# Performance work log

Hardware: AMD Instinct MI355X
Metric: run time of the kernel (lower is better)

The kernel has to match this reference:

```python
import jax, jax.numpy as jnp
import numpy as np

B, A, C, D = 64, 1024, 64, 512
NEG = -9.0e15


def _ln(x, w, b, eps=1e-5):
    mu = jnp.mean(x, axis=-1, keepdims=True)
    var = jnp.mean((x - mu) ** 2, axis=-1, keepdims=True)
    return (x - mu) * jax.lax.rsqrt(var + eps) * w + b


def setup_inputs() -> dict:
    key = jax.random.key(0)
    ks = jax.random.split(key, 8)
    att_index = np.arange(A) % C
    am = np.zeros((C, A), np.float32)
    am[att_index, np.arange(A)] = 1.0 / (A // C)  # avgmask[i,j]=1/count if att_index[j]==i
    adj_ha = np.concatenate([am, np.eye(C, dtype=np.float32)], axis=1)      # [C, A+C]
    adj_ah = np.concatenate([am.T, np.eye(A, dtype=np.float32)], axis=1)    # [A, C+A]
    w = lambda k: jax.random.normal(k, (D, D), jnp.float32) * 0.05
    ones, zeros = jnp.ones((D,), jnp.float32), jnp.zeros((D,), jnp.float32)
    return {
        "att_vf": jax.random.normal(ks[0], (B, A, D), jnp.float32) * 0.05,
        "avgmask": jnp.asarray(am), "adj_ha": jnp.asarray(adj_ha), "adj_ah": jnp.asarray(adj_ah),
        "l1_W_h2h": w(ks[1]), "l1_W_h2a": w(ks[2]),
        "l1_ln1_w": ones, "l1_ln1_b": zeros, "l1_ln2_w": ones, "l1_ln2_b": zeros,
        "l1_ln3_w": ones, "l1_ln3_b": zeros,
        "l2_W_a2h": w(ks[3]), "l2_W_h2h": w(ks[4]), "l2_W_h2a": w(ks[5]),
        "l2_ln1_w": ones, "l2_ln1_b": zeros, "l2_ln2_w": ones, "l2_ln2_b": zeros,
        "l2_ln3_w": ones, "l2_ln3_b": zeros,
    }


def _forward(att_vf, avgmask, adj_ha, adj_ah,
             l1_W_h2h, l1_W_h2a, l1_ln1_w, l1_ln1_b, l1_ln2_w, l1_ln2_b, l1_ln3_w, l1_ln3_b,
             l2_W_a2h, l2_W_h2h, l2_W_h2a, l2_ln1_w, l2_ln1_b, l2_ln2_w, l2_ln2_b, l2_ln3_w, l2_ln3_b):
    inv_sd = 1.0 / jnp.sqrt(jnp.float32(D))  # input_dim == h_dim == D

    def h2h(hl, W, lw, lb):
        hln = _ln(hl, lw, lb)                                  # [B,C,D]
        hide = hln @ W
        s = jnp.einsum('bid,bjd->bij', hide, hide) * inv_sd
        a = jax.nn.softmax(s, axis=-1)
        return jnp.einsum('bij,bjd->bid', a, hln)

    def h2a(upd_hl, att, W, lw, lb):
        hln = _ln(upd_hl, lw, lb)
        hidden = jnp.concatenate([hln @ W, att], axis=1)       # [B, C+A, D]
        s = jnp.einsum('bad,bkd->bak', att, hidden) * inv_sd   # [B, A, C+A]
        s = jnp.where(adj_ah > 0, s, NEG)
        a = jax.nn.softmax(s, axis=-1)
        return jnp.einsum('bak,bkd->bad', a, hidden)

    # layer 1: a2h = 'avg'
    hl = jnp.einsum('ca,bad->bcd', avgmask, _ln(att_vf, l1_ln1_w, l1_ln1_b))  # [B,C,D]
    hl1 = h2h(hl, l1_W_h2h, l1_ln2_w, l1_ln2_b)
    att1 = h2a(hl1, att_vf, l1_W_h2a, l1_ln3_w, l1_ln3_b)

    # layer 2: a2h = 'attention'
    att_ln = _ln(att1, l2_ln1_w, l2_ln1_b)
    hidden = jnp.concatenate([att_ln @ l2_W_a2h, hl1], axis=1)  # [B, A+C, D]
    s = jnp.einsum('bcd,bkd->bck', hl1, hidden) * inv_sd        # [B, C, A+C]
    s = jnp.where(adj_ha > 0, s, NEG)
    hl2 = jnp.einsum('bck,bkd->bcd', jax.nn.softmax(s, axis=-1), hidden)
    hl2 = h2h(hl2, l2_W_h2h, l2_ln2_w, l2_ln2_b)
    att2 = h2a(hl2, att1, l2_W_h2a, l2_ln3_w, l2_ln3_b)
    return att2


def reference(att_vf, avgmask, adj_ha, adj_ah,
              l1_W_h2h, l1_W_h2a, l1_ln1_w, l1_ln1_b, l1_ln2_w, l1_ln2_b, l1_ln3_w, l1_ln3_b,
              l2_W_a2h, l2_W_h2h, l2_W_h2a, l2_ln1_w, l2_ln1_b, l2_ln2_w, l2_ln2_b, l2_ln3_w, l2_ln3_b):
    return _forward(att_vf, avgmask, adj_ha, adj_ah,
                    l1_W_h2h, l1_W_h2a, l1_ln1_w, l1_ln1_b, l1_ln2_w, l1_ln2_b, l1_ln3_w, l1_ln3_b,
                    l2_W_a2h, l2_W_h2h, l2_W_h2a, l2_ln1_w, l2_ln1_b, l2_ln2_w, l2_ln2_b, l2_ln3_w, l2_ln3_b)
```

## Files before the change

kernel.cpp:

```cpp
#include <hip/hip_runtime.h>

#define B_ 64
#define A_ 1024
#define C_ 64
#define D_ 512
#define INV_SD 0.044194173824159216f

typedef __bf16 bf16_t;
typedef __bf16 bf16x8 __attribute__((ext_vector_type(8)));
typedef __bf16 bf16x2 __attribute__((ext_vector_type(2)));
typedef float f32x4 __attribute__((ext_vector_type(4)));

static __device__ __forceinline__ bf16_t f2b(float x) { return (bf16_t)x; }
static __device__ __forceinline__ float b2f(bf16_t x) { return (float)x; }

static __device__ __forceinline__ void gl_lds16(const void* g, void* l) {
  __builtin_amdgcn_global_load_lds(
      (const __attribute__((address_space(1))) unsigned int*)g,
      (__attribute__((address_space(3))) unsigned int*)l, 16, 0, 0);
}

__global__ __launch_bounds__(256) void k_prep(const float* __restrict__ att,
                                              const float* __restrict__ lw1,
                                              const float* __restrict__ lb1,
                                              const float* __restrict__ lw2,
                                              const float* __restrict__ lb2,
                                              bf16_t* __restrict__ hlnb,
                                              const float* __restrict__ W0,
                                              const float* __restrict__ W1,
                                              const float* __restrict__ W2,
                                              const float* __restrict__ W3,
                                              const float* __restrict__ W4,
                                              bf16_t* __restrict__ WtBase) {
  __shared__ float shm[64 * 65];
  __shared__ float reds[8];
  int bid = blockIdx.x;
  int t = threadIdx.x;
  if (bid < B_ * C_) {
    int b = bid >> 6, c = bid & 63;
    int w = t >> 6, lane = t & 63;
    float (*part)[512] = (float(*)[512])shm;
    float ps[8] = {0.f, 0.f, 0.f, 0.f, 0.f, 0.f, 0.f, 0.f};
#pragma unroll
    for (int i = 0; i < 4; ++i) {
      int jj = w * 4 + i;
      const float* xr = att + ((size_t)b * A_ + jj * 64 + c) * D_ + lane * 8;
      float4 v1 = *(const float4*)xr;
      float4 v2 = *(const float4*)(xr + 4);
      float v[8] = {v1.x, v1.y, v1.z, v1.w, v2.x, v2.y, v2.z, v2.w};
      float s = 0.f, q = 0.f;
#pragma unroll
      for (int u = 0; u < 8; ++u) { s += v[u]; q += v[u] * v[u]; }
#pragma unroll
      for (int o = 32; o; o >>= 1) { s += __shfl_xor(s, o); q += __shfl_xor(q, o); }
      float mu = s * (1.0f / D_);
      float rs = rsqrtf(q * (1.0f / D_) - mu * mu + 1e-5f);
#pragma unroll
      for (int u = 0; u < 8; ++u) ps[u] += (v[u] - mu) * rs;
    }
#pragma unroll
    for (int u = 0; u < 8; ++u) part[w][lane * 8 + u] = ps[u];
    __syncthreads();
    int d = 2 * t;
    float hx = ((part[0][d] + part[1][d]) + (part[2][d] + part[3][d])) * (1.f / 16.f) * lw1[d] + lb1[d];
    float hy = ((part[0][d + 1] + part[1][d + 1]) + (part[2][d + 1] + part[3][d + 1])) * (1.f / 16.f) * lw1[d + 1] + lb1[d + 1];
    float s = hx + hy, q = hx * hx + hy * hy;
#pragma unroll
    for (int o = 32; o; o >>= 1) { s += __shfl_xor(s, o); q += __shfl_xor(q, o); }
    if (lane == 0) { reds[w] = s; reds[4 + w] = q; }
    __syncthreads();
    float S = (reds[0] + reds[1]) + (reds[2] + reds[3]);
    float Q = (reds[4] + reds[5]) + (reds[6] + reds[7]);
    float mu = S * (1.0f / D_);
    float rs = rsqrtf(Q * (1.0f / D_) - mu * mu + 1e-5f);
    bf16x2 ob;
    ob.x = f2b((hx - mu) * rs * lw2[d] + lb2[d]);
    ob.y = f2b((hy - mu) * rs * lw2[d + 1] + lb2[d + 1]);
    *(bf16x2*)(hlnb + (size_t)bid * D_ + d) = ob;
  } else {
    int idx = bid - B_ * C_;
    int z = idx >> 6;
    int rem = idx & 63;
    int k0 = (rem & 7) * 64, n0 = (rem >> 3) * 64;
    const float* Ws[5] = {W0, W1, W2, W3, W4};
    int r0 = t >> 6;
    int c = t & 63;
    if (z == 5) {
      const float* W = Ws[2];
      bf16_t* Wt = WtBase + (size_t)5 * 512 * 512;
#pragma unroll 4
      for (int i = 0; i < 16; ++i) {
        int r = r0 * 16 + i;
        Wt[(size_t)(k0 + r) * 512 + n0 + c] = f2b(W[(size_t)(k0 + r) * 512 + n0 + c]);
      }
      return;
    }
    const float* W = Ws[z];
    bf16_t* Wt = WtBase + (size_t)z * 512 * 512;
    float (*tile)[65] = (float(*)[65])shm;
#pragma unroll 4
    for (int i = 0; i < 16; ++i) {
      int r = r0 * 16 + i;
      tile[r][c] = W[(size_t)(k0 + r) * 512 + n0 + c];
    }
    __syncthreads();
#pragma unroll 4
    for (int i = 0; i < 16; ++i) {
      int r = r0 * 16 + i;
      Wt[(size_t)(n0 + r) * 512 + k0 + c] = f2b(tile[c][r]);
    }
  }
}

__global__ __launch_bounds__(256) void k_ln_tr(const bf16_t* __restrict__ x,
                                               const float* __restrict__ lw,
                                               const float* __restrict__ lb,
                                               bf16_t* __restrict__ y,
                                               bf16_t* __restrict__ yt) {
  __shared__ bf16_t lnS[64][528];
  int b = blockIdx.x;
  int t = threadIdx.x;
  int wv = t >> 6, lane = t & 63;
  int d0 = lane * 8;
  float4 w1 = *(const float4*)(lw + d0);
  float4 w2 = *(const float4*)(lw + d0 + 4);
  float4 b1 = *(const float4*)(lb + d0);
  float4 b2 = *(const float4*)(lb + d0 + 4);
  float lwv[8] = {w1.x, w1.y, w1.z, w1.w, w2.x, w2.y, w2.z, w2.w};
  float lbv[8] = {b1.x, b1.y, b1.z, b1.w, b2.x, b2.y, b2.z, b2.w};
  const bf16_t* xb = x + (size_t)b * C_ * D_;
  bf16_t* yb = y + (size_t)b * C_ * D_;
#pragma unroll 4
  for (int i = 0; i < 16; ++i) {
    int r = wv * 16 + i;
    bf16x8 xv = *(const bf16x8*)(xb + (size_t)r * D_ + d0);
    float v[8], s = 0.f, q = 0.f;
#pragma unroll
    for (int u = 0; u < 8; ++u) { v[u] = b2f(xv[u]); s += v[u]; q += v[u] * v[u]; }
#pragma unroll
    for (int o = 32; o; o >>= 1) { s += __shfl_xor(s, o); q += __shfl_xor(q, o); }
    float mu = s * (1.0f / D_);
    float rs = rsqrtf(q * (1.0f / D_) - mu * mu + 1e-5f);
    bf16x8 ob;
#pragma unroll
    for (int u = 0; u < 8; ++u) ob[u] = f2b((v[u] - mu) * rs * lwv[u] + lbv[u]);
    *(bf16x8*)(yb + (size_t)r * D_ + d0) = ob;
    *(bf16x8*)(&lnS[r][d0]) = ob;
  }
  __syncthreads();
  bf16_t* tb = yt + (size_t)b * D_ * C_;
#pragma unroll
  for (int pass = 0; pass < 16; ++pass) {
    int d = pass * 32 + (t >> 3);
    int c0 = (t & 7) * 8;
    unsigned short tmp[8];
#pragma unroll
    for (int u = 0; u < 8; ++u) tmp[u] = *(const unsigned short*)&lnS[c0 + u][d];
    *(uint4*)(tb + (size_t)d * 64 + c0) = *(const uint4*)tmp;
  }
}

template <bool BIAS>
__global__ __launch_bounds__(256, 4) void k_gemm64(const bf16_t* __restrict__ A0,
                                                   const bf16_t* __restrict__ W0,
                                                   bf16_t* __restrict__ C0,
                                                   const bf16_t* __restrict__ A1,
                                                   const bf16_t* __restrict__ W1,
                                                   bf16_t* __restrict__ C1,
                                                   const bf16_t* __restrict__ Rb,
                                                   int tiles_per, int ntiles,
                                                   const bf16_t* __restrict__ trS,
                                                   bf16_t* __restrict__ trD) {
  constexpr int ABYTES = 64 * 128;
  constexpr int BUF = 2 * ABYTES;
  __shared__ char smem[2 * BUF];

  int t = threadIdx.x;
  int bid = blockIdx.x;

  if (bid >= ntiles) {
    int idx = bid - ntiles;
    int n0 = idx & 7, b = idx >> 3;
    unsigned short(*sm)[72] = (unsigned short(*)[72])smem;
    const bf16_t* sb = trS + (size_t)b * C_ * D_;
    bf16_t* db = trD + (size_t)b * D_ * C_;
#pragma unroll
    for (int rep = 0; rep < 2; ++rep) {
      int f = t + rep * 256;
      int r = f >> 3, c8 = f & 7;
      uint4 v = *(const uint4*)(sb + (size_t)r * D_ + n0 * 64 + c8 * 8);
      unsigned int* p = (unsigned int*)&sm[r][c8 * 8];
      p[0] = v.x; p[1] = v.y; p[2] = v.z; p[3] = v.w;
    }
    __syncthreads();
#pragma unroll
    for (int rep = 0; rep < 2; ++rep) {
      int f = t + rep * 256;
      int nr = f >> 3, c8 = f & 7;
      unsigned short tmp[8];
#pragma unroll
      for (int u = 0; u < 8; ++u) tmp[u] = sm[c8 * 8 + u][nr];
      *(uint4*)(db + (size_t)(n0 * 64 + nr) * 64 + c8 * 8) = *(const uint4*)tmp;
    }
    return;
  }

  int lane = t & 63, wave = t >> 6;
  int wr = wave >> 1, wc = wave & 1;
  int lhi = lane >> 4, llo = lane & 15;

  int tile = (bid & 7) * (ntiles >> 3) + (bid >> 3);
  int sel = (tile >= tiles_per) ? 1 : 0;
  int tidx = tile - sel * tiles_per;
  int bm = tidx >> 3, bn = tidx & 7;

  const bf16_t* Ab = (sel ? A1 : A0) + (size_t)bm * 64 * 512;
  const bf16_t* Wb = (sel ? W1 : W0) + (size_t)bn * 64 * 512;
  bf16_t* Cmat = sel ? C1 : C0;

  int l3 = lane >> 3;
  int srcOff = ((lane & 7) ^ l3) * 8;

  auto stage = [&](int k0, int bi) {
    char* As = smem + bi * BUF;
    char* Bs = As + ABYTES;
#pragma unroll
    for (int i = 0; i < 2; ++i) {
      int r0 = wave * 16 + i * 8;
      gl_lds16(Ab + (size_t)(r0 + l3) * 512 + k0 + srcOff, As + r0 * 128);
      gl_lds16(Wb + (size_t)(r0 + l3) * 512 + k0 + srcOff, Bs + r0 * 128);
    }
  };

  f32x4 acc[2][2] = {};
  stage(0, 0);
  __syncthreads();

  for (int it = 0; it < 8; ++it) {
    int cur = it & 1;
    if (it < 7) stage((it + 1) * 64, cur ^ 1);
    const char* As = smem + cur * BUF;
    const char* Bs = As + ABYTES;
#pragma unroll
    for (int kk = 0; kk < 2; ++kk) {
      bf16x8 af[2], bfr[2];
      int bofs = kk * 64 + lhi * 16;
#pragma unroll
      for (int tr = 0; tr < 2; ++tr) {
        int row = wr * 32 + tr * 16 + llo;
        af[tr] = *(const bf16x8*)(As + row * 128 + (bofs ^ ((row & 7) << 4)));
      }
#pragma unroll
      for (int tc = 0; tc < 2; ++tc) {
        int col = wc * 32 + tc * 16 + llo;
        bfr[tc] = *(const bf16x8*)(Bs + col * 128 + (bofs ^ ((col & 7) << 4)));
      }
#pragma unroll
      for (int tr = 0; tr < 2; ++tr)
#pragma unroll
        for (int tc = 0; tc < 2; ++tc)
          acc[tr][tc] = __builtin_amdgcn_mfma_f32_16x16x32_bf16(af[tr], bfr[tc], acc[tr][tc], 0, 0, 0);
    }
    __syncthreads();
  }

  bf16_t(*Cs)[80] = (bf16_t(*)[80])smem;
#pragma unroll
  for (int tr = 0; tr < 2; ++tr) {
    int row = wr * 32 + tr * 16 + lhi * 4;
#pragma unroll
    for (int r = 0; r < 4; ++r)
#pragma unroll
      for (int tc = 0; tc < 2; ++tc) {
        float v = acc[tr][tc][r];
        if constexpr (BIAS)
          v += b2f(Rb[(size_t)(bm * 64 + row + r) * 512 + bn * 64 + wc * 32 + tc * 16 + llo]);
        Cs[row + r][wc * 32 + tc * 16 + llo] = f2b(v);
      }
  }
  __syncthreads();
#pragma unroll
  for (int it = 0; it < 2; ++it) {
    int idx = t + it * 256;
    int row = idx >> 3, c8 = idx & 7;
    uint4 v = *(const uint4*)(&Cs[row][c8 * 8]);
    *(uint4*)(Cmat + (size_t)(bm * 64 + row) * 512 + bn * 64 + c8 * 8) = v;
  }
}

template <int MODE>
__global__ __launch_bounds__(256) void k_h2h(const bf16_t* __restrict__ hide,
                                             const bf16_t* __restrict__ hlnT,
                                             const float* __restrict__ lnw,
                                             const float* __restrict__ lnbv,
                                             float* __restrict__ hl1f,
                                             bf16_t* __restrict__ hl1b,
                                             bf16_t* __restrict__ lnout) {
  __shared__ bf16_t hS[8 * 64 * 64];
  __shared__ float sS[16][68];
  __shared__ bf16_t wS[16 * 64];
  __shared__ float mur[16], rsr[16];

  int q = blockIdx.x;
  int b = blockIdx.y;
  int t = threadIdx.x;
  int lane = t & 63, wave = t >> 6;
  int lhi = lane >> 4, llo = lane & 15;

  const bf16_t* Hb = hide + (size_t)b * C_ * D_;
#pragma unroll
  for (int rep = 0; rep < 16; ++rep) {
    int f = t + rep * 256;
    int row = f >> 6, c16 = f & 63;
    int kc = c16 >> 3, ci = c16 & 7;
    uint4 v = *(const uint4*)(Hb + (size_t)row * 512 + c16 * 8);
    *(uint4*)((char*)hS + kc * 8192 + row * 128 + ((ci * 16) ^ ((row & 7) << 4))) = v;
  }
  __syncthreads();

  {
    f32x4 acc = {};
#pragma unroll
    for (int ks = 0; ks < 16; ++ks) {
      int kc = ks >> 1;
      int bofs = (ks & 1) * 64 + lhi * 16;
      int ra = q * 16 + llo;
      int rb = wave * 16 + llo;
      bf16x8 af = *(const bf16x8*)((const char*)hS + kc * 8192 + ra * 128 + (bofs ^ ((ra & 7) << 4)));
      bf16x8 bf = *(const bf16x8*)((const char*)hS + kc * 8192 + rb * 128 + (bofs ^ ((rb & 7) << 4)));
      acc = __builtin_amdgcn_mfma_f32_16x16x32_bf16(af, bf, acc, 0, 0, 0);
    }
#pragma unroll
    for (int r = 0; r < 4; ++r) sS[lhi * 4 + r][wave * 16 + llo] = acc[r] * INV_SD;
  }
  __syncthreads();

  if (t < 128) {
    int row = t >> 3, sg = t & 7;
    float v[8];
#pragma unroll
    for (int u = 0; u < 8; ++u) v[u] = sS[row][sg * 8 + u];
    float m = v[0];
#pragma unroll
    for (int u = 1; u < 8; ++u) m = fmaxf(m, v[u]);
#pragma unroll
    for (int o = 4; o; o >>= 1) m = fmaxf(m, __shfl_xor(m, o));
    float sum = 0.f;
#pragma unroll
    for (int u = 0; u < 8; ++u) { v[u] = __expf(v[u] - m); sum += v[u]; }
#pragma unroll
    for (int o = 4; o; o >>= 1) sum += __shfl_xor(sum, o);
    float inv = 1.f / sum;
    bf16x8 wv;
#pragma unroll
    for (int u = 0; u < 8; ++u) wv[u] = f2b(v[u] * inv);
    *(bf16x8*)((char*)wS + row * 128 + ((sg * 16) ^ ((row & 7) << 4))) = wv;
  }
  __syncthreads();

  float* sf = (float*)hS;
  {
    bf16x8 af[2];
#pragma unroll
    for (int ks = 0; ks < 2; ++ks)
      af[ks] = *(const bf16x8*)((const char*)wS + llo * 128 + (((ks * 64 + lhi * 16)) ^ ((llo & 7) << 4)));
    const bf16_t* Tb = hlnT + (size_t)b * D_ * C_;
#pragma unroll
    for (int nt = 0; nt < 8; ++nt) {
      int dcol = wave * 128 + nt * 16 + llo;
      f32x4 acc = {};
#pragma unroll
      for (int ks = 0; ks < 2; ++ks) {
        bf16x8 bf = *(const bf16x8*)(Tb + (size_t)dcol * 64 + ks * 32 + lhi * 8);
        acc = __builtin_amdgcn_mfma_f32_16x16x32_bf16(af[ks], bf, acc, 0, 0, 0);
      }
#pragma unroll
      for (int r = 0; r < 4; ++r) sf[(lhi * 4 + r) * 516 + dcol] = acc[r];
    }
  }
  __syncthreads();

  {
    int lr = t >> 4, p = t & 15;
    float s = 0.f, q2 = 0.f;
#pragma unroll 8
    for (int i = 0; i < 32; ++i) {
      float v = sf[lr * 516 + p + 16 * i];
      s += v;
      q2 += v * v;
    }
#pragma unroll
    for (int o = 8; o; o >>= 1) { s += __shfl_xor(s, o); q2 += __shfl_xor(q2, o); }
    if (p == 0) {
      float mu = s * (1.0f / D_);
      mur[lr] = mu;
      rsr[lr] = rsqrtf(q2 * (1.0f / D_) - mu * mu + 1e-5f);
    }
  }
  __syncthreads();

  int d = 2 * t;
  float lwx = lnw[d], lwy = lnw[d + 1], lbx = lnbv[d], lby = lnbv[d + 1];
#pragma unroll 4
  for (int r = 0; r < 16; ++r) {
    float2 xy = *(const float2*)(&sf[r * 516 + d]);
    size_t go = ((size_t)b * C_ + q * 16 + r) * 512 + d;
    float mu = mur[r], rs = rsr[r];
    if constexpr (MODE == 0) {
      *(float2*)(hl1f + go) = xy;
      bf16x2 hb;
      hb.x = f2b(xy.x);
      hb.y = f2b(xy.y);
      *(bf16x2*)(hl1b + go) = hb;
    }
    bf16x2 lb2;
    lb2.x = f2b((xy.x - mu) * rs * lwx + lbx);
    lb2.y = f2b((xy.y - mu) * rs * lwy + lby);
    *(bf16x2*)(lnout + go) = lb2;
  }
}

__global__ __launch_bounds__(256) void k_l2head(const float* __restrict__ att,
                                                const bf16_t* __restrict__ hW,
                                                const float* __restrict__ hl1f,
                                                const bf16_t* __restrict__ G,
                                                const float* __restrict__ lw,
                                                const float* __restrict__ lb,
                                                bf16_t* __restrict__ att1b,
                                                bf16_t* __restrict__ u_out,
                                                bf16_t* __restrict__ R_out) {
  int blk = blockIdx.x;
  int b = blk >> 6, c = blk & 63;
  int t = threadIdx.x;
  int w = t >> 6, lane = t & 63;
  int d0 = lane * 8;
  __shared__ bf16_t lnS[16][512];
  __shared__ float hrow[512];
  __shared__ float wts[32];
  __shared__ float red[4];

  {
    int d = 2 * t;
    float2 h2 = *(const float2*)(hl1f + (size_t)blk * 512 + d);
    hrow[d] = h2.x;
    hrow[d + 1] = h2.y;
    float sd = h2.x * h2.x + h2.y * h2.y;
#pragma unroll
    for (int o = 32; o; o >>= 1) sd += __shfl_xor(sd, o);
    if (lane == 0) red[w] = sd;
  }
  bf16x8 wb = *(const bf16x8*)(hW + (size_t)blk * 512 + d0);
  bf16x8 gb = *(const bf16x8*)(G + (size_t)blk * 512 + d0);
  float wv[8], gv[8];
#pragma unroll
  for (int u = 0; u < 8; ++u) { wv[u] = b2f(wb[u]); gv[u] = b2f(gb[u]); }
  float4 w1 = *(const float4*)(lw + d0);
  float4 w2 = *(const float4*)(lw + d0 + 4);
  float4 b1 = *(const float4*)(lb + d0);
  float4 b2 = *(const float4*)(lb + d0 + 4);
  float lwv[8] = {w1.x, w1.y, w1.z, w1.w, w2.x, w2.y, w2.z, w2.w};
  float lbv[8] = {b1.x, b1.y, b1.z, b1.w, b2.x, b2.y, b2.z, b2.w};

#pragma unroll
  for (int i = 0; i < 4; ++i) {
    int j = w * 4 + i;
    size_t row = (size_t)b * A_ + j * 64 + c;
    const float* ar = att + row * 512 + d0;
    float4 a1 = *(const float4*)ar;
    float4 a2 = *(const float4*)(ar + 4);
    float av[8] = {a1.x, a1.y, a1.z, a1.w, a2.x, a2.y, a2.z, a2.w};
    float d1 = 0.f, d2 = 0.f;
#pragma unroll
    for (int u = 0; u < 8; ++u) { d1 += av[u] * wv[u]; d2 += av[u] * av[u]; }
#pragma unroll
    for (int o = 32; o; o >>= 1) { d1 += __shfl_xor(d1, o); d2 += __shfl_xor(d2, o); }
    float s1 = d1 * INV_SD, s2 = d2 * INV_SD;
    float m = fmaxf(s1, s2);
    float e1 = __expf(s1 - m), e2 = __expf(s2 - m);
    float inv = 1.f / (e1 + e2);
    float alpha = e1 * inv, beta = e2 * inv;
    float o8[8], s = 0.f, q = 0.f;
    bf16x8 ob;
#pragma unroll
    for (int u = 0; u < 8; ++u) {
      o8[u] = alpha * wv[u] + beta * av[u];
      s += o8[u];
      q += o8[u] * o8[u];
      ob[u] = f2b(o8[u]);
    }
    *(bf16x8*)(att1b + row * 512 + d0) = ob;
#pragma unroll
    for (int o = 32; o; o >>= 1) { s += __shfl_xor(s, o); q += __shfl_xor(q, o); }
    float mu = s * (1.0f / D_);
    float rs = rsqrtf(q * (1.0f / D_) - mu * mu + 1e-5f);
    float dot = 0.f;
    bf16x8 lnv;
#pragma unroll
    for (int u = 0; u < 8; ++u) {
      float v = (o8[u] - mu) * rs * lwv[u] + lbv[u];
      lnv[u] = f2b(v);
      dot += v * gv[u];
    }
    *(bf16x8*)(&lnS[j][d0]) = lnv;
#pragma unroll
    for (int o = 32; o; o >>= 1) dot += __shfl_xor(dot, o);
    if (lane == 0) wts[j] = dot * INV_SD;
  }
  __syncthreads();
  if (t == 0) wts[16] = ((red[0] + red[1]) + (red[2] + red[3])) * INV_SD;
  __syncthreads();
  if (t < 64) {
    float val = (t < 17) ? wts[t] : -3.0e38f;
    float m = val;
#pragma unroll
    for (int o = 32; o; o >>= 1) m = fmaxf(m, __shfl_xor(m, o));
    float e = (t < 17) ? __expf(val - m) : 0.f;
    float ssum = e;
#pragma unroll
    for (int o = 32; o; o >>= 1) ssum += __shfl_xor(ssum, o);
    if (t < 17) wts[t] = e / ssum;
  }
  __syncthreads();
  int d = 2 * t;
  float ux = 0.f, uy = 0.f;
#pragma unroll 4
  for (int jj = 0; jj < 16; ++jj) {
    bf16x2 l2 = *(const bf16x2*)(&lnS[jj][d]);
    ux += wts[jj] * b2f(l2.x);
    uy += wts[jj] * b2f(l2.y);
  }
  bf16x2 uo, ro;
  uo.x = f2b(ux);
  uo.y = f2b(uy);
  *(bf16x2*)(u_out + (size_t)blk * 512 + d) = uo;
  float w16 = wts[16];
  ro.x = f2b(w16 * hrow[d]);
  ro.y = f2b(w16 * hrow[d + 1]);
  *(bf16x2*)(R_out + (size_t)blk * 512 + d) = ro;
}

__global__ __launch_bounds__(256) void k_h2a_out(const bf16_t* __restrict__ att,
                                                 const bf16_t* __restrict__ hW,
                                                 float* __restrict__ outp) {
  int t = threadIdx.x;
  int row = blockIdx.x * 4 + (t >> 6);
  int lane = t & 63;
  int b = row >> 10, a = row & 1023;
  int c = a & 63;
  int d0 = lane * 8;
  bf16x8 ab = *(const bf16x8*)(att + (size_t)row * D_ + d0);
  bf16x8 wb = *(const bf16x8*)(hW + (size_t)(b * 64 + c) * D_ + d0);
  float av[8], w[8];
#pragma unroll
  for (int u = 0; u < 8; ++u) { av[u] = b2f(ab[u]); w[u] = b2f(wb[u]); }
  float d1 = 0.f, d2 = 0.f;
#pragma unroll
  for (int u = 0; u < 8; ++u) { d1 += av[u] * w[u]; d2 += av[u] * av[u]; }
#pragma unroll
  for (int o = 32; o; o >>= 1) { d1 += __shfl_xor(d1, o); d2 += __shfl_xor(d2, o); }
  float s1 = d1 * INV_SD, s2 = d2 * INV_SD;
  float m = fmaxf(s1, s2);
  float e1 = __expf(s1 - m), e2 = __expf(s2 - m);
  float inv = 1.f / (e1 + e2);
  float alpha = e1 * inv, beta = e2 * inv;
  float4 o1, o2;
  o1.x = alpha * w[0] + beta * av[0]; o1.y = alpha * w[1] + beta * av[1];
  o1.z = alpha * w[2] + beta * av[2]; o1.w = alpha * w[3] + beta * av[3];
  o2.x = alpha * w[4] + beta * av[4]; o2.y = alpha * w[5] + beta * av[5];
  o2.z = alpha * w[6] + beta * av[6]; o2.w = alpha * w[7] + beta * av[7];
  float* orow = outp + (size_t)row * D_ + d0;
  *(float4*)orow = o1;
  *(float4*)(orow + 4) = o2;
}

extern "C" void kernel_launch(void* const* d_in, const int* in_sizes, int n_in,
                              void* d_out, int out_size, void* d_ws, size_t ws_size,
                              hipStream_t stream) {
  const float* att_vf = (const float*)d_in[0];
  const float* W1_h2h = (const float*)d_in[4];
  const float* W1_h2a = (const float*)d_in[5];
  const float* ln11w = (const float*)d_in[6];
  const float* ln11b = (const float*)d_in[7];
  const float* ln12w = (const float*)d_in[8];
  const float* ln12b = (const float*)d_in[9];
  const float* ln13w = (const float*)d_in[10];
  const float* ln13b = (const float*)d_in[11];
  const float* W2_a2h = (const float*)d_in[12];
  const float* W2_h2h = (const float*)d_in[13];
  const float* W2_h2a = (const float*)d_in[14];
  const float* ln21w = (const float*)d_in[15];
  const float* ln21b = (const float*)d_in[16];
  const float* ln22w = (const float*)d_in[17];
  const float* ln22b = (const float*)d_in[18];
  const float* ln23w = (const float*)d_in[19];
  const float* ln23b = (const float*)d_in[20];
  float* out = (float*)d_out;

  float* ws = (float*)d_ws;
  const size_t SM = (size_t)B_ * C_ * D_;
  float* hl1f = ws;
  bf16_t* A1b = (bf16_t*)(hl1f + SM);
  bf16_t* A1t = (bf16_t*)((float*)A1b + SM / 2);
  bf16_t* A2b = (bf16_t*)((float*)A1t + SM / 2);
  bf16_t* hl1b = (bf16_t*)((float*)A2b + SM / 2);
  bf16_t* u_b = (bf16_t*)((float*)hl1b + SM / 2);
  bf16_t* R_b = (bf16_t*)((float*)u_b + SM / 2);
  bf16_t* Gb = (bf16_t*)((float*)R_b + SM / 2);
  bf16_t* Wt0 = (bf16_t*)((float*)Gb + SM / 2);
  const size_t WTE = (size_t)512 * 512;
  bf16_t* att1b = Wt0 + 6 * WTE;

  dim3 blk(256);
  k_prep<<<B_ * C_ + 384, blk, 0, stream>>>(att_vf, ln11w, ln11b, ln12w, ln12b, A1b,
                                            W1_h2h, W1_h2a, W2_a2h, W2_h2h, W2_h2a, Wt0);
  k_gemm64<false><<<1024, blk, 0, stream>>>(A1b, Wt0 + 0 * WTE, A2b,
                                            A1b, Wt0 + 0 * WTE, A2b, nullptr, 512, 512,
                                            A1b, A1t);
  k_h2h<0><<<dim3(4, B_), blk, 0, stream>>>(A2b, A1t, ln13w, ln13b, hl1f, hl1b, A1b);
  k_gemm64<false><<<1024, blk, 0, stream>>>(A1b, Wt0 + 1 * WTE, A2b,
                                            hl1b, Wt0 + 5 * WTE, Gb, nullptr, 512, 1024,
                                            nullptr, nullptr);
  k_l2head<<<B_ * C_, blk, 0, stream>>>(att_vf, A2b, hl1f, Gb, ln21w, ln21b, att1b, u_b, R_b);
  k_gemm64<true><<<512, blk, 0, stream>>>(u_b, Wt0 + 2 * WTE, A2b,
                                          u_b, Wt0 + 2 * WTE, A2b, R_b, 512, 512,
                                          nullptr, nullptr);
  k_ln_tr<<<B_, blk, 0, stream>>>(A2b, ln22w, ln22b, A1b, A1t);
  k_gemm64<false><<<512, blk, 0, stream>>>(A1b, Wt0 + 3 * WTE, A2b,
                                           A1b, Wt0 + 3 * WTE, A2b, nullptr, 512, 512,
                                           nullptr, nullptr);
  k_h2h<1><<<dim3(4, B_), blk, 0, stream>>>(A2b, A1t, ln23w, ln23b, nullptr, nullptr, A1b);
  k_gemm64<false><<<512, blk, 0, stream>>>(A1b, Wt0 + 4 * WTE, A2b,
                                           A1b, Wt0 + 4 * WTE, A2b, nullptr, 512, 512,
                                           nullptr, nullptr);
  k_h2a_out<<<(B_ * A_) / 4, blk, 0, stream>>>(att1b, A2b, out);
}
```

Baseline: 180.5 us.

## Widen GEMM K-tile to 128 and hoist row loads ahead of reductions

The 64x64 GEMM now stages K in chunks of 128 instead of 64. That halves the main-loop iterations and barriers, and it needs a new 256-byte-row XOR swizzle plus double the LDS, so occupancy is lowered to 2 blocks per CU. In the prep and h2a kernels, all four input rows are loaded into registers before the per-row reductions start, so more global loads are in flight at once. The cost is higher register and LDS pressure.

Result: slower. 184.6 us (+2.3%).

```diff
diff --git a/kernel.cpp b/kernel.cpp
--- a/kernel.cpp
+++ b/kernel.cpp
@@ -40,23 +40,28 @@
     int b = bid >> 6, c = bid & 63;
     int w = t >> 6, lane = t & 63;
     float (*part)[512] = (float(*)[512])shm;
-    float ps[8] = {0.f, 0.f, 0.f, 0.f, 0.f, 0.f, 0.f, 0.f};
+    float vv[4][8];
 #pragma unroll
     for (int i = 0; i < 4; ++i) {
       int jj = w * 4 + i;
       const float* xr = att + ((size_t)b * A_ + jj * 64 + c) * D_ + lane * 8;
       float4 v1 = *(const float4*)xr;
       float4 v2 = *(const float4*)(xr + 4);
-      float v[8] = {v1.x, v1.y, v1.z, v1.w, v2.x, v2.y, v2.z, v2.w};
+      vv[i][0] = v1.x; vv[i][1] = v1.y; vv[i][2] = v1.z; vv[i][3] = v1.w;
+      vv[i][4] = v2.x; vv[i][5] = v2.y; vv[i][6] = v2.z; vv[i][7] = v2.w;
+    }
+    float ps[8] = {0.f, 0.f, 0.f, 0.f, 0.f, 0.f, 0.f, 0.f};
+#pragma unroll
+    for (int i = 0; i < 4; ++i) {
       float s = 0.f, q = 0.f;
 #pragma unroll
-      for (int u = 0; u < 8; ++u) { s += v[u]; q += v[u] * v[u]; }
+      for (int u = 0; u < 8; ++u) { s += vv[i][u]; q += vv[i][u] * vv[i][u]; }
 #pragma unroll
       for (int o = 32; o; o >>= 1) { s += __shfl_xor(s, o); q += __shfl_xor(q, o); }
       float mu = s * (1.0f / D_);
       float rs = rsqrtf(q * (1.0f / D_) - mu * mu + 1e-5f);
 #pragma unroll
-      for (int u = 0; u < 8; ++u) ps[u] += (v[u] - mu) * rs;
+      for (int u = 0; u < 8; ++u) ps[u] += (vv[i][u] - mu) * rs;
     }
 #pragma unroll
     for (int u = 0; u < 8; ++u) part[w][lane * 8 + u] = ps[u];
@@ -67,7 +72,8 @@
     float s = hx + hy, q = hx * hx + hy * hy;
 #pragma unroll
     for (int o = 32; o; o >>= 1) { s += __shfl_xor(s, o); q += __shfl_xor(q, o); }
-    if (lane == 0) { reds[w] = s; reds[4 + w] = q; }
+    int lane2 = t & 63, w2 = t >> 6;
+    if (lane2 == 0) { reds[w2] = s; reds[4 + w2] = q; }
     __syncthreads();
     float S = (reds[0] + reds[1]) + (reds[2] + reds[3]);
     float Q = (reds[4] + reds[5]) + (reds[6] + reds[7]);
@@ -161,7 +167,7 @@
 }
 
 template <bool BIAS>
-__global__ __launch_bounds__(256, 4) void k_gemm64(const bf16_t* __restrict__ A0,
+__global__ __launch_bounds__(256, 2) void k_gemm64(const bf16_t* __restrict__ A0,
                                                    const bf16_t* __restrict__ W0,
                                                    bf16_t* __restrict__ C0,
                                                    const bf16_t* __restrict__ A1,
@@ -171,8 +177,8 @@
                                                    int tiles_per, int ntiles,
                                                    const bf16_t* __restrict__ trS,
                                                    bf16_t* __restrict__ trD) {
-  constexpr int ABYTES = 64 * 128;
-  constexpr int BUF = 2 * ABYTES;
+  constexpr int MATB = 64 * 256;
+  constexpr int BUF = 2 * MATB;
   __shared__ char smem[2 * BUF];
 
   int t = threadIdx.x;
@@ -218,17 +224,17 @@
   const bf16_t* Wb = (sel ? W1 : W0) + (size_t)bn * 64 * 512;
   bf16_t* Cmat = sel ? C1 : C0;
 
-  int l3 = lane >> 3;
-  int srcOff = ((lane & 7) ^ l3) * 8;
+  int lrow = lane >> 4;
 
   auto stage = [&](int k0, int bi) {
     char* As = smem + bi * BUF;
-    char* Bs = As + ABYTES;
-#pragma unroll
-    for (int i = 0; i < 2; ++i) {
-      int r0 = wave * 16 + i * 8;
-      gl_lds16(Ab + (size_t)(r0 + l3) * 512 + k0 + srcOff, As + r0 * 128);
-      gl_lds16(Wb + (size_t)(r0 + l3) * 512 + k0 + srcOff, Bs + r0 * 128);
+    char* Bs = As + MATB;
+#pragma unroll
+    for (int i = 0; i < 4; ++i) {
+      int r0 = wave * 16 + i * 4;
+      int srcOff = ((lane & 15) ^ (i * 4 + lrow)) * 8;
+      gl_lds16(Ab + (size_t)(r0 + lrow) * 512 + k0 + srcOff, As + r0 * 256);
+      gl_lds16(Wb + (size_t)(r0 + lrow) * 512 + k0 + srcOff, Bs + r0 * 256);
     }
   };
 
@@ -236,24 +242,24 @@
   stage(0, 0);
   __syncthreads();
 
-  for (int it = 0; it < 8; ++it) {
+  for (int it = 0; it < 4; ++it) {
     int cur = it & 1;
-    if (it < 7) stage((it + 1) * 64, cur ^ 1);
+    if (it < 3) stage((it + 1) * 128, cur ^ 1);
     const char* As = smem + cur * BUF;
-    const char* Bs = As + ABYTES;
-#pragma unroll
-    for (int kk = 0; kk < 2; ++kk) {
+    const char* Bs = As + MATB;
+#pragma unroll
+    for (int kk = 0; kk < 4; ++kk) {
       bf16x8 af[2], bfr[2];
       int bofs = kk * 64 + lhi * 16;
 #pragma unroll
       for (int tr = 0; tr < 2; ++tr) {
         int row = wr * 32 + tr * 16 + llo;
-        af[tr] = *(const bf16x8*)(As + row * 128 + (bofs ^ ((row & 7) << 4)));
+        af[tr] = *(const bf16x8*)(As + row * 256 + (bofs ^ ((row & 15) << 4)));
       }
 #pragma unroll
       for (int tc = 0; tc < 2; ++tc) {
         int col = wc * 32 + tc * 16 + llo;
-        bfr[tc] = *(const bf16x8*)(Bs + col * 128 + (bofs ^ ((col & 7) << 4)));
+        bfr[tc] = *(const bf16x8*)(Bs + col * 256 + (bofs ^ ((col & 15) << 4)));
       }
 #pragma unroll
       for (int tr = 0; tr < 2; ++tr)
@@ -461,17 +467,24 @@
   float lwv[8] = {w1.x, w1.y, w1.z, w1.w, w2.x, w2.y, w2.z, w2.w};
   float lbv[8] = {b1.x, b1.y, b1.z, b1.w, b2.x, b2.y, b2.z, b2.w};
 
+  float av4[4][8];
+#pragma unroll
+  for (int i = 0; i < 4; ++i) {
+    int j = w * 4 + i;
+    const float* ar = att + ((size_t)b * A_ + j * 64 + c) * 512 + d0;
+    float4 a1 = *(const float4*)ar;
+    float4 a2 = *(const float4*)(ar + 4);
+    av4[i][0] = a1.x; av4[i][1] = a1.y; av4[i][2] = a1.z; av4[i][3] = a1.w;
+    av4[i][4] = a2.x; av4[i][5] = a2.y; av4[i][6] = a2.z; av4[i][7] = a2.w;
+  }
+
 #pragma unroll
   for (int i = 0; i < 4; ++i) {
     int j = w * 4 + i;
     size_t row = (size_t)b * A_ + j * 64 + c;
-    const float* ar = att + row * 512 + d0;
-    float4 a1 = *(const float4*)ar;
-    float4 a2 = *(const float4*)(ar + 4);
-    float av[8] = {a1.x, a1.y, a1.z, a1.w, a2.x, a2.y, a2.z, a2.w};
     float d1 = 0.f, d2 = 0.f;
 #pragma unroll
-    for (int u = 0; u < 8; ++u) { d1 += av[u] * wv[u]; d2 += av[u] * av[u]; }
+    for (int u = 0; u < 8; ++u) { d1 += av4[i][u] * wv[u]; d2 += av4[i][u] * av4[i][u]; }
 #pragma unroll
     for (int o = 32; o; o >>= 1) { d1 += __shfl_xor(d1, o); d2 += __shfl_xor(d2, o); }
     float s1 = d1 * INV_SD, s2 = d2 * INV_SD;
@@ -483,7 +496,7 @@
     bf16x8 ob;
 #pragma unroll
     for (int u = 0; u < 8; ++u) {
-      o8[u] = alpha * wv[u] + beta * av[u];
+      o8[u] = alpha * wv[u] + beta * av4[i][u];
       s += o8[u];
       q += o8[u] * o8[u];
       ob[u] = f2b(o8[u]);
```
